# Performance work log

Hardware: AMD Instinct MI355X
Metric: run time of the kernel (lower is better)

The kernel has to match this reference:

```python
import jax, jax.numpy as jnp
import numpy as np

B, C, H, W = 8, 512, 128, 128
WS = 8

def _proj(x, w, b):
    # 1x1 conv == channel GEMM: (B,C,H,W) x (Cout,Cin) -> (B,Cout,H,W)
    return jnp.einsum('bchw,oc->bohw', x, w) + b[None, :, None, None]

def _split_windows(x):
    # (B,C,H,W) -> (B*nH*nW, ws*ws, C)
    b, c, h, w = x.shape
    x = x.reshape(b, c, h // WS, WS, w // WS, WS)
    x = x.transpose(0, 2, 4, 3, 5, 1)
    return x.reshape(-1, WS * WS, c)

def _merge_windows(x, b, c, h, w):
    # (B*nH*nW, ws*ws, C) -> (B,C,H,W)
    x = x.reshape(b, h // WS, w // WS, WS, WS, c)
    x = x.transpose(0, 5, 1, 3, 2, 4)
    return x.reshape(b, c, h, w)

def setup_inputs() -> dict:
    key = jax.random.key(0)
    ks = jax.random.split(key, 9)
    s = 1.0 / np.sqrt(C)
    return {
        'x': jax.random.normal(ks[0], (B, C, H, W), jnp.float32),
        'wq': jax.random.normal(ks[1], (C, C), jnp.float32) * s,
        'bq': jnp.zeros((C,), jnp.float32),
        'wk': jax.random.normal(ks[2], (C, C), jnp.float32) * s,
        'bk': jnp.zeros((C,), jnp.float32),
        'wv': jax.random.normal(ks[3], (C, C), jnp.float32) * s,
        'bv': jnp.zeros((C,), jnp.float32),
        'wo': jax.random.normal(ks[4], (C, C), jnp.float32) * s,
        'bo': jnp.zeros((C,), jnp.float32),
    }

def reference(x, wq, bq, wk, bk, wv, bv, wo, bo):
    b, c, h, w = x.shape
    q = _split_windows(_proj(x, wq, bq))  # (nWin, ws*ws, C)
    k = _split_windows(_proj(x, wk, bk))
    v = _split_windows(_proj(x, wv, bv))
    attn = jnp.einsum('nqc,nkc->nqk', q, k) / jnp.sqrt(jnp.asarray(c, x.dtype))
    attn = jax.nn.softmax(attn, axis=-1)
    out = jnp.einsum('nqk,nkc->nqc', attn, v)
    out = _merge_windows(out, b, c, h, w)
    return _proj(out, wo, bo)
```

## Files before the change

### kernel.cpp

```cpp
#include <hip/hip_runtime.h>

typedef __attribute__((ext_vector_type(8))) short bf16x8;
typedef __attribute__((ext_vector_type(4))) float f32x4;

#define MFMA16(a, b, c) __builtin_amdgcn_mfma_f32_16x16x32_bf16((a), (b), (c), 0, 0, 0)

__device__ __forceinline__ float b2f(unsigned short u) {
  unsigned int v = ((unsigned int)u) << 16;
  return __builtin_bit_cast(float, v);
}
__device__ __forceinline__ unsigned short f2b(float f) {
  unsigned int u = __builtin_bit_cast(unsigned int, f);
  u += 0x7fffu + ((u >> 16) & 1u);
  return (unsigned short)(u >> 16);
}
__device__ __forceinline__ void gload16(const void* g, void* l) {
  __builtin_amdgcn_global_load_lds(
      (const __attribute__((address_space(1))) unsigned int*)g,
      (__attribute__((address_space(3))) unsigned int*)l, 16, 0, 0);
}

__global__ __launch_bounds__(256) void k_wconv(
    const float* __restrict__ src, unsigned short* __restrict__ dst) {
  const int i = (blockIdx.x * 256 + threadIdx.x) * 4;
  const float4 v = *(const float4*)(src + i);
  uint2 p;
  p.x = (unsigned int)f2b(v.x) | ((unsigned int)f2b(v.y) << 16);
  p.y = (unsigned int)f2b(v.z) | ((unsigned int)f2b(v.w) << 16);
  *(uint2*)(dst + i) = p;
}

__global__ __launch_bounds__(256) void k_wtrans(
    const float* __restrict__ in, unsigned short* __restrict__ out) {
  __shared__ unsigned short tile[64][72];
  const int r0 = blockIdx.x << 6, s0 = blockIdx.y << 6;
  const int t = threadIdx.x;
  {
    const int sl = t >> 3, rl = (t & 7) << 3;
#pragma unroll
    for (int pass = 0; pass < 2; ++pass) {
      const int s = sl + pass * 32;
      const float* src = in + (size_t)(s0 + s) * 512 + r0 + rl;
      const float4 f0 = ((const float4*)src)[0];
      const float4 f1 = ((const float4*)src)[1];
      tile[rl + 0][s] = f2b(f0.x);
      tile[rl + 1][s] = f2b(f0.y);
      tile[rl + 2][s] = f2b(f0.z);
      tile[rl + 3][s] = f2b(f0.w);
      tile[rl + 4][s] = f2b(f1.x);
      tile[rl + 5][s] = f2b(f1.y);
      tile[rl + 6][s] = f2b(f1.z);
      tile[rl + 7][s] = f2b(f1.w);
    }
  }
  __syncthreads();
  {
    const int rl = t >> 3, sl = (t & 7) << 3;
#pragma unroll
    for (int pass = 0; pass < 2; ++pass) {
      const int r = rl + pass * 32;
      uint4 v = *(const uint4*)&tile[r][sl];
      *(uint4*)(out + (size_t)(r0 + r) * 512 + s0 + sl) = v;
    }
  }
}

__global__ __launch_bounds__(256) void k_bvo(
    const float* __restrict__ wo, const float* __restrict__ bv,
    const float* __restrict__ bo, float* __restrict__ bvo) {
  const int o = blockIdx.x * 256 + threadIdx.x;
  float acc = bo[o];
  const float* row = wo + (size_t)o * 512;
  for (int j = 0; j < 512; ++j) acc += row[j] * bv[j];
  bvo[o] = acc;
}

__global__ __launch_bounds__(256) void k_ub(
    const float* __restrict__ wk, const float* __restrict__ bq,
    float* __restrict__ u) {
  const int c = blockIdx.x * 256 + threadIdx.x;
  float acc = 0.f;
  for (int o = 0; o < 512; ++o) acc += bq[o] * wk[(size_t)o * 512 + c];
  u[c] = acc;
}

__global__ __launch_bounds__(256) void k_transpose(
    const float* __restrict__ X, unsigned short* __restrict__ XT,
    unsigned short* __restrict__ XV) {
  const int bx = blockIdx.x;
  const int wt = bx & 1, ht = bx >> 1;
  const int c0 = blockIdx.y << 5;
  const int b = blockIdx.z;
  const int w0 = wt << 6, h0 = ht << 3;
  const int t = threadIdx.x;
  const int cg = t & 3, pg = t >> 2;
  const int wi = pg >> 3, hh = pg & 7;
  const int h = h0 + hh, w = w0 + wi * 8;
  const int cbase = c0 + cg * 8;

  const float* xsrc = X + (size_t)b * 8388608u + (size_t)cbase * 16384 +
                      (size_t)h * 128 + w;
  float f[8][8];
#pragma unroll
  for (int ci = 0; ci < 8; ++ci) {
    const float4 a0 = ((const float4*)(xsrc + (size_t)ci * 16384))[0];
    const float4 a1 = ((const float4*)(xsrc + (size_t)ci * 16384))[1];
    f[ci][0] = a0.x; f[ci][1] = a0.y; f[ci][2] = a0.z; f[ci][3] = a0.w;
    f[ci][4] = a1.x; f[ci][5] = a1.y; f[ci][6] = a1.z; f[ci][7] = a1.w;
  }

  unsigned short* xtdst =
      XT + (size_t)b * 8388608u + ((size_t)h * 128 + w) * 512 + cbase;
#pragma unroll
  for (int pi = 0; pi < 8; ++pi) {
    unsigned short o[8];
#pragma unroll
    for (int ci = 0; ci < 8; ++ci) o[ci] = f2b(f[ci][pi]);
    *(uint4*)(xtdst + (size_t)pi * 512) = *(const uint4*)o;
  }

  const int win = b * 256 + ht * 16 + wt * 8 + wi;
  unsigned short* xvdst =
      XV + (size_t)cbase * 131072 + (size_t)win * 64 + hh * 8;
#pragma unroll
  for (int ci = 0; ci < 8; ++ci) {
    unsigned short o[8];
#pragma unroll
    for (int pi = 0; pi < 8; ++pi) o[pi] = f2b(f[ci][pi]);
    *(uint4*)(xvdst + (size_t)ci * 131072) = *(const uint4*)o;
  }
}

template <int MODE>
__global__ __launch_bounds__(512, 2) void k_gemm256(
    const unsigned short* __restrict__ A, const unsigned short* __restrict__ B,
    const float* __restrict__ bias0, void* __restrict__ C0v) {
  __shared__ unsigned short lsA[4][256 * 32];
  __shared__ unsigned short lsB[4][256 * 32];
  const int bid = blockIdx.x;
  int mt, nt;
  if (MODE == 0) {
    const int work = ((bid & 7) << 7) + (bid >> 3);
    mt = work >> 1; nt = work & 1;
  } else if (MODE == 2) {
    const int work = ((bid & 7) << 7) + (bid >> 3);
    nt = work >> 1; mt = work & 1;
  } else {
    mt = bid & 1; nt = bid >> 1;
  }
  const int m0 = mt << 8, n0 = nt << 8;

  const int t = threadIdx.x;
  const int l = t & 63;
  const int lr = l & 15, lg = l >> 4;
  const int w = t >> 6;
  const int wr = w >> 2, wc = w & 3;
  const int ra = wr << 7, rb = wc << 6;
  const int srowS = t >> 2;
  const int scolS = (t & 3) << 3;

  f32x4 acc[8][4];
#pragma unroll
  for (int i = 0; i < 8; ++i)
#pragma unroll
    for (int j = 0; j < 4; ++j) acc[i][j] = f32x4{0.f, 0.f, 0.f, 0.f};

  auto stage = [&](int kt) {
    const int buf = kt & 3, k0 = kt << 5;
#pragma unroll
    for (int hh = 0; hh < 2; ++hh) {
      gload16(A + (size_t)(m0 + srowS + hh * 128) * 512 + k0 + scolS,
              &lsA[buf][(srowS + hh * 128) * 32 + scolS]);
      gload16(B + (size_t)(n0 + srowS + hh * 128) * 512 + k0 + scolS,
              &lsB[buf][(srowS + hh * 128) * 32 + scolS]);
    }
  };
  auto compute = [&](int kt) {
    const int buf = kt & 3;
    bf16x8 af[8], bfv[4];
#pragma unroll
    for (int i = 0; i < 8; ++i)
      af[i] = *(const bf16x8*)&lsA[buf][(ra + i * 16 + lr) * 32 + lg * 8];
#pragma unroll
    for (int j = 0; j < 4; ++j)
      bfv[j] = *(const bf16x8*)&lsB[buf][(rb + j * 16 + lr) * 32 + lg * 8];
    __builtin_amdgcn_s_setprio(1);
#pragma unroll
    for (int i = 0; i < 8; ++i)
#pragma unroll
      for (int j = 0; j < 4; ++j)
        acc[i][j] = MFMA16(af[i], bfv[j], acc[i][j]);
    __builtin_amdgcn_s_setprio(0);
  };

  stage(0); stage(1); stage(2);

#define GITER(kt, vm)                                        \
  asm volatile("s_waitcnt vmcnt(" #vm ")" ::: "memory");     \
  __builtin_amdgcn_s_barrier();                              \
  __builtin_amdgcn_sched_barrier(0);                         \
  if ((kt) + 3 < 16) stage((kt) + 3);                        \
  compute(kt);                                               \
  __builtin_amdgcn_sched_barrier(0);                         \
  __builtin_amdgcn_s_barrier();

  GITER(0, 8)  GITER(1, 8)  GITER(2, 8)  GITER(3, 8)
  GITER(4, 8)  GITER(5, 8)  GITER(6, 8)  GITER(7, 8)
  GITER(8, 8)  GITER(9, 8)  GITER(10, 8) GITER(11, 8)
  GITER(12, 8) GITER(13, 8) GITER(14, 4) GITER(15, 0)
#undef GITER

#pragma unroll
  for (int i = 0; i < 8; ++i) {
    const int cmb = m0 + ra + i * 16 + lg * 4;
#pragma unroll
    for (int j = 0; j < 4; ++j) {
      const int cn = n0 + rb + j * 16 + lr;
      const float bn = (MODE == 0) ? bias0[cn] : 0.f;
#pragma unroll
      for (int r = 0; r < 4; ++r) {
        const int cm = cmb + r;
        if (MODE == 0) {
          ((unsigned short*)C0v)[(size_t)cm * 512 + cn] = f2b(acc[i][j][r] + bn);
        } else if (MODE == 2) {
          const float val = acc[i][j][r] + bias0[cm];
          const int bb = cn >> 14, p = cn & 16383;
          ((float*)C0v)[(size_t)bb * 8388608 + (size_t)cm * 16384 + p] = val;
        } else {
          ((unsigned short*)C0v)[(size_t)cm * 512 + cn] = f2b(acc[i][j][r]);
        }
      }
    }
  }
}

__global__ __launch_bounds__(256) void k_attn(
    const unsigned short* __restrict__ Q, const unsigned short* __restrict__ XT,
    const unsigned short* __restrict__ XV, unsigned short* __restrict__ Y) {
  __shared__ unsigned short P_lds[4][64][72];
  const int t = threadIdx.x, w = t >> 6, l = t & 63;
  const int lr = l & 15, lg = l >> 4;
  const int grp = ((blockIdx.x & 7) << 6) + (blockIdx.x >> 3);
  const int win = grp * 4 + w;
  const int b = win >> 8, th = (win >> 4) & 15, tw = win & 15;
  const size_t p_base = (size_t)b * 16384 + (size_t)th * 1024 + (size_t)tw * 8;
  const size_t rowpix = p_base + (size_t)(lr >> 3) * 128 + (lr & 7);
  const unsigned short* qbase = Q + rowpix * 512;
  const unsigned short* kbase = XT + rowpix * 512;

  f32x4 acc[4][4];
#pragma unroll
  for (int i = 0; i < 4; ++i)
#pragma unroll
    for (int j = 0; j < 4; ++j) acc[i][j] = f32x4{0.f, 0.f, 0.f, 0.f};

  bf16x8 kp[2][4], qp[2][4];
#pragma unroll
  for (int pp = 0; pp < 2; ++pp) {
    const int co = pp * 32 + lg * 8;
#pragma unroll
    for (int i = 0; i < 4; ++i) {
      kp[pp][i] = *(const bf16x8*)(kbase + (size_t)i * 131072 + co);
      qp[pp][i] = *(const bf16x8*)(qbase + (size_t)i * 131072 + co);
    }
  }
#pragma unroll
  for (int cs = 0; cs < 16; ++cs) {
    const int cb = cs & 1;
    __builtin_amdgcn_s_setprio(1);
#pragma unroll
    for (int mt = 0; mt < 4; ++mt)
#pragma unroll
      for (int qt = 0; qt < 4; ++qt)
        acc[mt][qt] = MFMA16(kp[cb][mt], qp[cb][qt], acc[mt][qt]);
    __builtin_amdgcn_s_setprio(0);
    if (cs + 2 < 16) {
      const int co = (cs + 2) * 32 + lg * 8;
#pragma unroll
      for (int i = 0; i < 4; ++i) {
        kp[cb][i] = *(const bf16x8*)(kbase + (size_t)i * 131072 + co);
        qp[cb][i] = *(const bf16x8*)(qbase + (size_t)i * 131072 + co);
      }
    }
  }

  const float scale = 0.044194173824159216f;
#pragma unroll
  for (int qt = 0; qt < 4; ++qt) {
    float pv[4][4];
    float mx = -3.0e38f;
#pragma unroll
    for (int mt = 0; mt < 4; ++mt)
#pragma unroll
      for (int j = 0; j < 4; ++j) {
        const float s = acc[mt][qt][j] * scale;
        pv[mt][j] = s;
        mx = fmaxf(mx, s);
      }
    mx = fmaxf(mx, __shfl_xor(mx, 16));
    mx = fmaxf(mx, __shfl_xor(mx, 32));
    float sum = 0.f;
#pragma unroll
    for (int mt = 0; mt < 4; ++mt)
#pragma unroll
      for (int j = 0; j < 4; ++j) {
        const float e = __expf(pv[mt][j] - mx);
        pv[mt][j] = e;
        sum += e;
      }
    sum += __shfl_xor(sum, 16);
    sum += __shfl_xor(sum, 32);
    const float inv = 1.f / sum;
#pragma unroll
    for (int mt = 0; mt < 4; ++mt)
#pragma unroll
      for (int j = 0; j < 4; j += 2) {
        const unsigned int pk =
            (unsigned int)f2b(pv[mt][j] * inv) |
            ((unsigned int)f2b(pv[mt][j + 1] * inv) << 16);
        *(unsigned int*)&P_lds[w][qt * 16 + lr][mt * 16 + lg * 4 + j] = pk;
      }
  }

  bf16x8 pa0[4], pa1[4];
#pragma unroll
  for (int qt = 0; qt < 4; ++qt) {
    pa0[qt] = *(const bf16x8*)&P_lds[w][qt * 16 + lr][lg * 8];
    pa1[qt] = *(const bf16x8*)&P_lds[w][qt * 16 + lr][32 + lg * 8];
  }
  const unsigned short* vbase =
      XV + (size_t)lr * 131072 + (size_t)win * 64 + lg * 8;
  unsigned short* ystore =
      Y + (p_base + (size_t)(lg >> 1) * 128 + ((lg & 1) << 2)) * 512 + lr;

  bf16x8 v0p[2], v1p[2];
#pragma unroll
  for (int pp = 0; pp < 2; ++pp) {
    const unsigned short* vp = vbase + (size_t)pp * (16 * 131072);
    v0p[pp] = *(const bf16x8*)vp;
    v1p[pp] = *(const bf16x8*)(vp + 32);
  }
#pragma unroll
  for (int nt = 0; nt < 32; ++nt) {
    const int cb = nt & 1;
    f32x4 o[4];
    __builtin_amdgcn_s_setprio(1);
#pragma unroll
    for (int qt = 0; qt < 4; ++qt) {
      o[qt] = f32x4{0.f, 0.f, 0.f, 0.f};
      o[qt] = MFMA16(pa0[qt], v0p[cb], o[qt]);
      o[qt] = MFMA16(pa1[qt], v1p[cb], o[qt]);
    }
    __builtin_amdgcn_s_setprio(0);
    if (nt + 2 < 32) {
      const unsigned short* vp = vbase + (size_t)(nt + 2) * (16 * 131072);
      v0p[cb] = *(const bf16x8*)vp;
      v1p[cb] = *(const bf16x8*)(vp + 32);
    }
#pragma unroll
    for (int qt = 0; qt < 4; ++qt)
#pragma unroll
      for (int r = 0; r < 4; ++r)
        ystore[(size_t)qt * 131072 + r * 512 + nt * 16] = f2b(o[qt][r]);
  }
}

extern "C" void kernel_launch(void* const* d_in, const int* in_sizes, int n_in,
                              void* d_out, int out_size, void* d_ws,
                              size_t ws_size, hipStream_t stream) {
  (void)in_sizes; (void)n_in; (void)out_size;
  const float* x = (const float*)d_in[0];
  const float* wq = (const float*)d_in[1];
  const float* bq = (const float*)d_in[2];
  const float* wk = (const float*)d_in[3];
  const float* bk = (const float*)d_in[4];
  const float* wv = (const float*)d_in[5];
  const float* bv = (const float*)d_in[6];
  const float* wo = (const float*)d_in[7];
  const float* bo = (const float*)d_in[8];
  (void)bk;

  const size_t NEED = (size_t)(2097152 + 3 * 67108864) * 2;
  if (ws_size < NEED) return;

  unsigned short* wb = (unsigned short*)d_ws;
  unsigned short* wqT = wb;
  unsigned short* wkT = wb + 262144;
  unsigned short* wvT = wb + 524288;
  unsigned short* wo_b = wb + 786432;
  unsigned short* wvo = wb + 1048576;
  float* bvo = (float*)(wb + 1310720);
  float* ub = (float*)(wb + 1311744);
  unsigned short* Bqk = wb + 1572864;
  unsigned short* xT = wb + 2097152;
  unsigned short* xV = xT + 67108864;
  unsigned short* Ybuf = xV + 67108864;
  unsigned short* Tq = (unsigned short*)d_out;

  k_wtrans<<<dim3(8, 8), 256, 0, stream>>>(wq, wqT);
  k_wtrans<<<dim3(8, 8), 256, 0, stream>>>(wk, wkT);
  k_wtrans<<<dim3(8, 8), 256, 0, stream>>>(wv, wvT);
  k_wconv<<<256, 256, 0, stream>>>(wo, wo_b);
  k_gemm256<3><<<4, 512, 0, stream>>>(wkT, wqT, nullptr, Bqk);
  k_gemm256<3><<<4, 512, 0, stream>>>(wo_b, wvT, nullptr, wvo);
  k_ub<<<2, 256, 0, stream>>>(wk, bq, ub);
  k_bvo<<<2, 256, 0, stream>>>(wo, bv, bo, bvo);
  k_transpose<<<dim3(32, 16, 8), 256, 0, stream>>>(x, xT, xV);
  k_gemm256<0><<<1024, 512, 0, stream>>>(xT, Bqk, ub, Tq);
  k_attn<<<512, 256, 0, stream>>>(Tq, xT, xV, Ybuf);
  k_gemm256<2><<<1024, 512, 0, stream>>>(wvo, Ybuf, bvo, d_out);
}
```

Measured before the change: 583.5 us.

## Swizzle GEMM LDS layout, remap transpose threads, merge small prep kernels

Adds an XOR swizzle to the GEMM LDS tiles. The global source column is permuted at load time and the reads use the matching offset, which is meant to remove LDS bank conflicts on the fragment reads. The x transpose kernel is remapped so each block covers 4 full rows of 128 pixels, giving more contiguous global reads. The three weight transposes are merged into one launch, as are the two bias kernels, to cut launch overhead. The swizzle must stay consistent between the loads and the reads, and it changes the global access pattern within each 64-byte segment.

```diff
diff --git a/kernel.cpp b/kernel.cpp
--- a/kernel.cpp
+++ b/kernel.cpp
@@ -30,9 +30,13 @@
   *(uint2*)(dst + i) = p;
 }
 
-__global__ __launch_bounds__(256) void k_wtrans(
-    const float* __restrict__ in, unsigned short* __restrict__ out) {
+__global__ __launch_bounds__(256) void k_wtrans3(
+    const float* __restrict__ wq, const float* __restrict__ wk,
+    const float* __restrict__ wv, unsigned short* __restrict__ outbase) {
   __shared__ unsigned short tile[64][72];
+  const int z = blockIdx.z;
+  const float* in = (z == 0) ? wq : (z == 1) ? wk : wv;
+  unsigned short* out = outbase + (size_t)z * 262144u;
   const int r0 = blockIdx.x << 6, s0 = blockIdx.y << 6;
   const int t = threadIdx.x;
   {
@@ -65,41 +69,40 @@
   }
 }
 
-__global__ __launch_bounds__(256) void k_bvo(
+__global__ __launch_bounds__(256) void k_bias(
     const float* __restrict__ wo, const float* __restrict__ bv,
-    const float* __restrict__ bo, float* __restrict__ bvo) {
-  const int o = blockIdx.x * 256 + threadIdx.x;
-  float acc = bo[o];
-  const float* row = wo + (size_t)o * 512;
-  for (int j = 0; j < 512; ++j) acc += row[j] * bv[j];
-  bvo[o] = acc;
-}
-
-__global__ __launch_bounds__(256) void k_ub(
-    const float* __restrict__ wk, const float* __restrict__ bq,
+    const float* __restrict__ bo, const float* __restrict__ wk,
+    const float* __restrict__ bq, float* __restrict__ bvo,
     float* __restrict__ u) {
-  const int c = blockIdx.x * 256 + threadIdx.x;
-  float acc = 0.f;
-  for (int o = 0; o < 512; ++o) acc += bq[o] * wk[(size_t)o * 512 + c];
-  u[c] = acc;
+  const int bid = blockIdx.x;
+  if (bid < 2) {
+    const int o = bid * 256 + threadIdx.x;
+    float acc = bo[o];
+    const float* row = wo + (size_t)o * 512;
+    for (int j = 0; j < 512; ++j) acc += row[j] * bv[j];
+    bvo[o] = acc;
+  } else {
+    const int c = (bid - 2) * 256 + threadIdx.x;
+    float acc = 0.f;
+    for (int o = 0; o < 512; ++o) acc += bq[o] * wk[(size_t)o * 512 + c];
+    u[c] = acc;
+  }
 }
 
 __global__ __launch_bounds__(256) void k_transpose(
     const float* __restrict__ X, unsigned short* __restrict__ XT,
     unsigned short* __restrict__ XV) {
-  const int bx = blockIdx.x;
-  const int wt = bx & 1, ht = bx >> 1;
+  const int hz = blockIdx.x;
   const int c0 = blockIdx.y << 5;
   const int b = blockIdx.z;
-  const int w0 = wt << 6, h0 = ht << 3;
+  const int h0 = hz << 2;
   const int t = threadIdx.x;
-  const int cg = t & 3, pg = t >> 2;
-  const int wi = pg >> 3, hh = pg & 7;
-  const int h = h0 + hh, w = w0 + wi * 8;
-  const int cbase = c0 + cg * 8;
-
-  const float* xsrc = X + (size_t)b * 8388608u + (size_t)cbase * 16384 +
-                      (size_t)h * 128 + w;
+  const int cg = t >> 6, hh = (t >> 4) & 3, wl = t & 15;
+  const int c8 = c0 + cg * 8;
+  const int h = h0 + hh;
+
+  const float* xsrc = X + (size_t)b * 8388608u + (size_t)c8 * 16384 +
+                      (size_t)h * 128 + wl * 8;
   float f[8][8];
 #pragma unroll
   for (int ci = 0; ci < 8; ++ci) {
@@ -110,7 +113,7 @@
   }
 
   unsigned short* xtdst =
-      XT + (size_t)b * 8388608u + ((size_t)h * 128 + w) * 512 + cbase;
+      XT + (size_t)b * 8388608u + ((size_t)h * 128 + wl * 8) * 512 + c8;
 #pragma unroll
   for (int pi = 0; pi < 8; ++pi) {
     unsigned short o[8];
@@ -119,9 +122,10 @@
     *(uint4*)(xtdst + (size_t)pi * 512) = *(const uint4*)o;
   }
 
-  const int win = b * 256 + ht * 16 + wt * 8 + wi;
+  const int win = b * 256 + (h0 >> 3) * 16 + wl;
+  const int hrow = h & 7;
   unsigned short* xvdst =
-      XV + (size_t)cbase * 131072 + (size_t)win * 64 + hh * 8;
+      XV + (size_t)c8 * 131072 + (size_t)win * 64 + hrow * 8;
 #pragma unroll
   for (int ci = 0; ci < 8; ++ci) {
     unsigned short o[8];
@@ -158,6 +162,10 @@
   const int ra = wr << 7, rb = wc << 6;
   const int srowS = t >> 2;
   const int scolS = (t & 3) << 3;
+  const int ssw = ((srowS >> 1) & 3) << 3;
+  const int scolX = scolS ^ ssw;
+  const int rsw = (lr >> 1) & 3;
+  const int rco = (lg ^ rsw) * 8;
 
   f32x4 acc[8][4];
 #pragma unroll
@@ -169,9 +177,9 @@
     const int buf = kt & 3, k0 = kt << 5;
 #pragma unroll
     for (int hh = 0; hh < 2; ++hh) {
-      gload16(A + (size_t)(m0 + srowS + hh * 128) * 512 + k0 + scolS,
+      gload16(A + (size_t)(m0 + srowS + hh * 128) * 512 + k0 + scolX,
               &lsA[buf][(srowS + hh * 128) * 32 + scolS]);
-      gload16(B + (size_t)(n0 + srowS + hh * 128) * 512 + k0 + scolS,
+      gload16(B + (size_t)(n0 + srowS + hh * 128) * 512 + k0 + scolX,
               &lsB[buf][(srowS + hh * 128) * 32 + scolS]);
     }
   };
@@ -180,10 +188,10 @@
     bf16x8 af[8], bfv[4];
 #pragma unroll
     for (int i = 0; i < 8; ++i)
-      af[i] = *(const bf16x8*)&lsA[buf][(ra + i * 16 + lr) * 32 + lg * 8];
+      af[i] = *(const bf16x8*)&lsA[buf][(ra + i * 16 + lr) * 32 + rco];
 #pragma unroll
     for (int j = 0; j < 4; ++j)
-      bfv[j] = *(const bf16x8*)&lsB[buf][(rb + j * 16 + lr) * 32 + lg * 8];
+      bfv[j] = *(const bf16x8*)&lsB[buf][(rb + j * 16 + lr) * 32 + rco];
     __builtin_amdgcn_s_setprio(1);
 #pragma unroll
     for (int i = 0; i < 8; ++i)
@@ -385,7 +393,6 @@
 
   unsigned short* wb = (unsigned short*)d_ws;
   unsigned short* wqT = wb;
-  unsigned short* wkT = wb + 262144;
   unsigned short* wvT = wb + 524288;
   unsigned short* wo_b = wb + 786432;
   unsigned short* wvo = wb + 1048576;
@@ -397,14 +404,11 @@
   unsigned short* Ybuf = xV + 67108864;
   unsigned short* Tq = (unsigned short*)d_out;
 
-  k_wtrans<<<dim3(8, 8), 256, 0, stream>>>(wq, wqT);
-  k_wtrans<<<dim3(8, 8), 256, 0, stream>>>(wk, wkT);
-  k_wtrans<<<dim3(8, 8), 256, 0, stream>>>(wv, wvT);
+  k_wtrans3<<<dim3(8, 8, 3), 256, 0, stream>>>(wq, wk, wv, wqT);
   k_wconv<<<256, 256, 0, stream>>>(wo, wo_b);
-  k_gemm256<3><<<4, 512, 0, stream>>>(wkT, wqT, nullptr, Bqk);
+  k_bias<<<4, 256, 0, stream>>>(wo, bv, bo, wk, bq, bvo, ub);
+  k_gemm256<3><<<4, 512, 0, stream>>>(wqT + 262144, wqT, nullptr, Bqk);
   k_gemm256<3><<<4, 512, 0, stream>>>(wo_b, wvT, nullptr, wvo);
-  k_ub<<<2, 256, 0, stream>>>(wk, bq, ub);
-  k_bvo<<<2, 256, 0, stream>>>(wo, bv, bo, bvo);
   k_transpose<<<dim3(32, 16, 8), 256, 0, stream>>>(x, xT, xV);
   k_gemm256<0><<<1024, 512, 0, stream>>>(xT, Bqk, ub, Tq);
   k_attn<<<512, 256, 0, stream>>>(Tq, xT, xV, Ybuf);
```

New measurement: 565.5 us. 3.1% less time.
